# Performance work log

Hardware: AMD Instinct MI355X
Metric: run time of the kernel (lower is better)

The kernel has to match this reference:

```python
import jax, jax.numpy as jnp
import numpy as np

V = 128      # vocab size (pad=0, sos=1, eos=2)
E = 128      # embed_dim == LSTM hidden
L = 2        # rnn_layers
B = 8192     # batch (num_samples)
T = 128      # token sequence length incl. sos/eos
PAD, SOS, EOS = 0, 1, 2


def setup_inputs() -> dict:
    key = jax.random.key(0)
    ks = jax.random.split(key, 9)
    s = 1.0 / np.sqrt(E)
    state = jax.random.normal(ks[0], (B, E), dtype=jnp.float32)
    tokens = jax.random.randint(ks[1], (B, T), 3, V)
    tokens = tokens.at[:, 0].set(SOS).at[:, -1].set(EOS)
    tok_embed = jax.random.normal(ks[2], (V, E), dtype=jnp.float32)
    W_ih = jax.random.uniform(ks[3], (L, 4 * E, E), minval=-s, maxval=s, dtype=jnp.float32)
    W_hh = jax.random.uniform(ks[4], (L, 4 * E, E), minval=-s, maxval=s, dtype=jnp.float32)
    b_ih = jax.random.uniform(ks[5], (L, 4 * E), minval=-s, maxval=s, dtype=jnp.float32)
    b_hh = jax.random.uniform(ks[6], (L, 4 * E), minval=-s, maxval=s, dtype=jnp.float32)
    W_out = jax.random.uniform(ks[7], (V, E), minval=-s, maxval=s, dtype=jnp.float32)
    b_out = jax.random.uniform(ks[8], (V,), minval=-s, maxval=s, dtype=jnp.float32)
    return {"state": state, "tokens": tokens, "tok_embed": tok_embed,
            "W_ih": W_ih, "W_hh": W_hh, "b_ih": b_ih, "b_hh": b_hh,
            "W_out": W_out, "b_out": b_out}


def _lstm(x, h0, c0, W_ih, W_hh, b_ih, b_hh):
    # x: [T, B, E] time-major; h0/c0: [L, B, E]. Gate order i,f,g,o (torch).
    n_layers = W_ih.shape[0]
    hs, cs = [], []
    for l in range(n_layers):
        Wih, Whh = W_ih[l], W_hh[l]
        b = b_ih[l] + b_hh[l]
        def step(carry, xt, Wih=Wih, Whh=Whh, b=b):
            h, c = carry
            g = xt @ Wih.T + h @ Whh.T + b            # [B, 4E]
            i, f, gg, o = jnp.split(g, 4, axis=-1)
            c = jax.nn.sigmoid(f) * c + jax.nn.sigmoid(i) * jnp.tanh(gg)
            h = jax.nn.sigmoid(o) * jnp.tanh(c)
            return (h, c), h
        (h, c), x = jax.lax.scan(step, (h0[l], c0[l]), x)
        hs.append(h)
        cs.append(c)
    return x, jnp.stack(hs), jnp.stack(cs)


def reference(state, tokens, tok_embed, W_ih, W_hh, b_ih, b_hh, W_out, b_out):
    b, e = state.shape
    n_layers = W_ih.shape[0]
    zeros = jnp.zeros((n_layers, b, e), dtype=state.dtype)
    # get_init_state: one-step LSTM over state.unsqueeze(0)
    _, h0, c0 = _lstm(state[None], zeros, zeros, W_ih, W_hh, b_ih, b_hh)
    # get_likelihood (all sequences same length -> dense, no pad tokens)
    x = tok_embed[tokens.T]                               # [T, B, E]
    out, _, _ = _lstm(x, h0, c0, W_ih, W_hh, b_ih, b_hh)  # [T, B, E]
    logits = out[:-1] @ W_out.T + b_out                   # [T-1, B, V]
    targets = tokens.T[1:]                                # [T-1, B]
    lp = jax.nn.log_softmax(logits, axis=-1)
    nll = -jnp.take_along_axis(lp, targets[..., None], axis=-1)[..., 0]
    mask = (targets != PAD).astype(nll.dtype)             # ignore_index=pad
    ll = -jnp.sum(nll * mask, axis=0)[:, None]            # [B, 1]
    return ll
```

## Files before the change

kernel.cpp:

```cpp
#include <hip/hip_runtime.h>
#include <hip/hip_bf16.h>


typedef __bf16 bf16x8 __attribute__((ext_vector_type(8)));
typedef __bf16 bf16x4 __attribute__((ext_vector_type(4)));
typedef float  f32x4  __attribute__((ext_vector_type(4)));

#define LOG2E 1.4426950408889634f
#define LN2   0.6931471805599453f

static __device__ __bf16 g_emb1[128 * 512];
static __device__ __bf16 g_woutbf[128 * 128];
static __device__ __bf16 g_wih2bf[512 * 128];
static __device__ __bf16 g_h1[(size_t)128 * 8192 * 128];

__device__ __forceinline__ float frcp(float x) {
#if __has_builtin(__builtin_amdgcn_rcpf)
  return __builtin_amdgcn_rcpf(x);
#else
  return 1.0f / x;
#endif
}
__device__ __forceinline__ float fexp2(float x) {
#if __has_builtin(__builtin_amdgcn_exp2f)
  return __builtin_amdgcn_exp2f(x);
#else
  return exp2f(x);
#endif
}
__device__ __forceinline__ float flog2(float x) {
#if __has_builtin(__builtin_amdgcn_logf)
  return __builtin_amdgcn_logf(x);
#else
  return log2f(x);
#endif
}

__device__ __forceinline__ int hoff(int row, int e) {
  return row * 128 + ((e + ((row & 15) << 3)) & 127);
}

__global__ void prep_emb1(const float* __restrict__ emb, const float* __restrict__ Wih,
                          const float* __restrict__ bih, const float* __restrict__ bhh,
                          const float* __restrict__ Wout) {
  __shared__ float embS[128 * 128];
  __shared__ float wS[32 * 128];
  const int tid = threadIdx.x, bc = blockIdx.x;
  for (int i = tid; i < 128 * 32; i += 512) ((f32x4*)embS)[i] = ((const f32x4*)emb)[i];
  for (int i = tid; i < 32 * 32; i += 512)
    ((f32x4*)wS)[i] = ((const f32x4*)(Wih + bc * 32 * 128))[i];
  {
    int idx = bc * 512 + tid;
    g_woutbf[idx * 2]     = (__bf16)(Wout[idx * 2] * LOG2E);
    g_woutbf[idx * 2 + 1] = (__bf16)(Wout[idx * 2 + 1] * LOG2E);
  }
  for (int i = bc * 512 + tid; i < 512 * 128; i += 16 * 512) {
    int gate = (i >> 14) & 3;
    float sc = (gate == 2) ? 2.0f * LOG2E : LOG2E;
    g_wih2bf[i] = (__bf16)(Wih[512 * 128 + i] * sc);
  }
  __syncthreads();
  const int v = tid & 127, c0 = (tid >> 7) * 8;
  const int rot = v & 31;
#pragma unroll
  for (int j = 0; j < 8; ++j) {
    int c = c0 + j;
    float s = 0.f;
    for (int k = 0; k < 128; ++k) {
      int kk = (k + rot) & 127;
      s += embS[v * 128 + kk] * wS[c * 128 + kk];
    }
    int col = bc * 32 + c;
    float sc = ((col >> 7) == 2) ? 2.0f * LOG2E : LOG2E;
    g_emb1[v * 512 + col] = (__bf16)((s + bih[col] + bhh[col]) * sc);
  }
}

__global__ __launch_bounds__(512, 2) void lstm_l1(
    const float* __restrict__ state, const int* __restrict__ tokens,
    const float* __restrict__ W_ih, const float* __restrict__ W_hh,
    const float* __restrict__ b_ih, const float* __restrict__ b_hh) {
  __shared__ __align__(16) __bf16 whh1L[512 * 128];
  __shared__ __align__(16) __bf16 h1L[2][32 * 128];
  __shared__ unsigned char tokL[127][32];

  const int tid  = threadIdx.x;
  const int w    = tid >> 6;
  const int lane = tid & 63;
  const int lr   = lane & 15;
  const int lh   = lane >> 4;
  const int b0   = blockIdx.x * 32;
  const int col  = w * 16 + lr;
  const int koff = lh * 8;
  const int e0   = w * 16 + lh * 4;
  const float gscA[4] = {LOG2E, LOG2E, 2.0f * LOG2E, LOG2E};

  auto ldw8s = [&](const float* p, float sc) -> bf16x8 {
    f32x4 x0 = *(const f32x4*)p, x1 = *(const f32x4*)(p + 4);
    bf16x8 v;
#pragma unroll
    for (int j = 0; j < 4; ++j) { v[j] = (__bf16)(x0[j] * sc); v[4 + j] = (__bf16)(x1[j] * sc); }
    return v;
  };

  for (int i = tid; i < 512 * 16; i += 512) {
    int row = i >> 4, e = (i & 15) * 8;
    *(bf16x8*)(whh1L + hoff(row, e)) = ldw8s(W_hh + row * 128 + e, gscA[row >> 7]);
  }
  for (int i = tid; i < 127 * 32; i += 512) {
    int r = i & 31, t = i >> 5;
    tokL[t][r] = (unsigned char)tokens[(b0 + r) * 128 + t];
  }

  f32x4 acc[4][2];
  float c1[2][4] = {};

  auto ldB = [&](const __bf16* buf, int nf, int kc) -> bf16x8 {
    return *(const bf16x8*)(buf + hoff(nf * 16 + lr, kc * 32 + koff));
  };

  auto elem1 = [&](const f32x4* b4, __bf16* hout, __bf16* gout) {
#pragma unroll
    for (int nf = 0; nf < 2; ++nf) {
      bf16x4 hp;
#pragma unroll
      for (int j = 0; j < 4; ++j) {
        float gi = acc[0][nf][j] + b4[0][j];
        float gf = acc[1][nf][j] + b4[1][j];
        float gc = acc[2][nf][j] + b4[2][j];
        float go = acc[3][nf][j] + b4[3][j];
        float sf = frcp(1.f + fexp2(-gf));
        float si = frcp(1.f + fexp2(-gi));
        float tg = 1.f - 2.f * frcp(fexp2(gc) + 1.f);
        float cc = sf * c1[nf][j] + si * tg;
        c1[nf][j] = cc;
        float so = frcp(1.f + fexp2(-go));
        float tc = 1.f - 2.f * frcp(fexp2(2.f * LOG2E * cc) + 1.f);
        hp[j] = (__bf16)(so * tc);
      }
      int b = nf * 16 + lr;
      *(bf16x4*)(hout + hoff(b, e0)) = hp;
      *(bf16x4*)(gout + (size_t)(b0 + b) * 128 + e0) = hp;
    }
  };
  const f32x4 zf4 = {0.f, 0.f, 0.f, 0.f};
  const f32x4 zb4[4] = {zf4, zf4, zf4, zf4};

  __syncthreads();

  bf16x4 gv[2][4];
  auto gather = [&](int t) {
#pragma unroll
    for (int nf = 0; nf < 2; ++nf) {
      int tk = (int)tokL[t][nf * 16 + lr];
      const __bf16* pp = g_emb1 + tk * 512 + e0;
#pragma unroll
      for (int gg = 0; gg < 4; ++gg) gv[nf][gg] = *(const bf16x4*)(pp + gg * 128);
    }
  };
  gather(0);

  {
#pragma unroll
    for (int gg = 0; gg < 4; ++gg)
#pragma unroll
      for (int nf = 0; nf < 2; ++nf) acc[gg][nf] = zf4;
#pragma unroll
    for (int kc = 0; kc < 4; ++kc) {
      bf16x8 s0 = ldw8s(state + (size_t)(b0 + lr) * 128 + kc * 32 + koff, 1.0f);
      bf16x8 s1 = ldw8s(state + (size_t)(b0 + 16 + lr) * 128 + kc * 32 + koff, 1.0f);
#pragma unroll
      for (int gg = 0; gg < 4; ++gg) {
        bf16x8 a = ldw8s(W_ih + (gg * 128 + col) * 128 + kc * 32 + koff, gscA[gg]);
        acc[gg][0] = __builtin_amdgcn_mfma_f32_16x16x32_bf16(a, s0, acc[gg][0], 0, 0, 0);
        acc[gg][1] = __builtin_amdgcn_mfma_f32_16x16x32_bf16(a, s1, acc[gg][1], 0, 0, 0);
      }
    }
    f32x4 bias1v4[4];
#pragma unroll
    for (int gg = 0; gg < 4; ++gg)
#pragma unroll
      for (int j = 0; j < 4; ++j)
        bias1v4[gg][j] = (b_ih[gg * 128 + e0 + j] + b_hh[gg * 128 + e0 + j]) * gscA[gg];
    elem1(bias1v4, h1L[0], g_h1);
    __syncthreads();
  }

#pragma unroll 1
  for (int t = 0; t < 127; ++t) {
    const __bf16* h1p = h1L[t & 1];
    __bf16* h1c = h1L[(t & 1) ^ 1];
#pragma unroll
    for (int gg = 0; gg < 4; ++gg)
#pragma unroll
      for (int nf = 0; nf < 2; ++nf)
#pragma unroll
        for (int j = 0; j < 4; ++j) acc[gg][nf][j] = (float)gv[nf][gg][j];
#pragma unroll
    for (int kc = 0; kc < 4; ++kc) {
      bf16x8 p0 = ldB(h1p, 0, kc), p1 = ldB(h1p, 1, kc);
#pragma unroll
      for (int gg = 0; gg < 4; ++gg) {
        bf16x8 a = *(const bf16x8*)(whh1L + hoff(gg * 128 + col, kc * 32 + koff));
        acc[gg][0] = __builtin_amdgcn_mfma_f32_16x16x32_bf16(a, p0, acc[gg][0], 0, 0, 0);
        acc[gg][1] = __builtin_amdgcn_mfma_f32_16x16x32_bf16(a, p1, acc[gg][1], 0, 0, 0);
      }
    }
    if (t + 1 < 127) gather(t + 1);
    elem1(zb4, h1c, g_h1 + (size_t)(t + 1) * 8192 * 128);
    __syncthreads();
  }
}

__global__ __launch_bounds__(512, 2) void lstm_l2(
    const int* __restrict__ tokens, const float* __restrict__ W_hh,
    const float* __restrict__ b_ih, const float* __restrict__ b_hh,
    const float* __restrict__ b_out, float* __restrict__ out) {
  __shared__ __align__(16) __bf16 whh2L[512 * 128];
  __shared__ __align__(16) __bf16 h1S[32 * 128];
  __shared__ __align__(16) __bf16 h2L[2][32 * 128];
  __shared__ unsigned char tokL[128][32];
  __shared__ float wsum[8][32];
  __shared__ float llL[32];

  const int tid  = threadIdx.x;
  const int w    = tid >> 6;
  const int lane = tid & 63;
  const int lr   = lane & 15;
  const int lh   = lane >> 4;
  const int b0   = blockIdx.x * 32;
  const int col  = w * 16 + lr;
  const int koff = lh * 8;
  const int e0   = w * 16 + lh * 4;
  const float gscA[4] = {LOG2E, LOG2E, 2.0f * LOG2E, LOG2E};

  auto ldw8s = [&](const float* p, float sc) -> bf16x8 {
    f32x4 x0 = *(const f32x4*)p, x1 = *(const f32x4*)(p + 4);
    bf16x8 v;
#pragma unroll
    for (int j = 0; j < 4; ++j) { v[j] = (__bf16)(x0[j] * sc); v[4 + j] = (__bf16)(x1[j] * sc); }
    return v;
  };

  for (int i = tid; i < 512 * 16; i += 512) {
    int row = i >> 4, e = (i & 15) * 8;
    *(bf16x8*)(whh2L + hoff(row, e)) = ldw8s(W_hh + 512 * 128 + row * 128 + e, gscA[row >> 7]);
  }
  for (int i = tid; i < 128 * 32; i += 512) {
    int r = i & 31, t = i >> 5;
    tokL[t][r] = (unsigned char)tokens[(b0 + r) * 128 + t];
  }
  if (tid < 32) llL[tid] = 0.0f;

  auto stageH1 = [&](int slot) {
    const __bf16* src = g_h1 + (size_t)slot * 8192 * 128 + (size_t)b0 * 128;
    int r = tid >> 4, e = (tid & 15) * 8;
    bf16x8 v = *(const bf16x8*)(src + r * 128 + e);
    *(bf16x8*)(h1S + hoff(r, e)) = v;
  };
  stageH1(0);

  f32x4 bias2v4[4], bo4;
#pragma unroll
  for (int gg = 0; gg < 4; ++gg)
#pragma unroll
    for (int j = 0; j < 4; ++j)
      bias2v4[gg][j] = (b_ih[512 + gg * 128 + e0 + j] + b_hh[512 + gg * 128 + e0 + j]) * gscA[gg];
#pragma unroll
  for (int j = 0; j < 4; ++j) bo4[j] = b_out[e0 + j] * LOG2E;

  float c2[2][4] = {};
  f32x4 acc[4][2];

  auto ldB = [&](const __bf16* buf, int nf, int kc) -> bf16x8 {
    return *(const bf16x8*)(buf + hoff(nf * 16 + lr, kc * 32 + koff));
  };

  auto elem2 = [&](__bf16* hout) {
#pragma unroll
    for (int nf = 0; nf < 2; ++nf) {
      bf16x4 hp;
#pragma unroll
      for (int j = 0; j < 4; ++j) {
        float gi = acc[0][nf][j] + bias2v4[0][j];
        float gf = acc[1][nf][j] + bias2v4[1][j];
        float gc = acc[2][nf][j] + bias2v4[2][j];
        float go = acc[3][nf][j] + bias2v4[3][j];
        float sf = frcp(1.f + fexp2(-gf));
        float si = frcp(1.f + fexp2(-gi));
        float tg = 1.f - 2.f * frcp(fexp2(gc) + 1.f);
        float cc = sf * c2[nf][j] + si * tg;
        c2[nf][j] = cc;
        float so = frcp(1.f + fexp2(-go));
        float tc = 1.f - 2.f * frcp(fexp2(2.f * LOG2E * cc) + 1.f);
        hp[j] = (__bf16)(so * tc);
      }
      int b = nf * 16 + lr;
      *(bf16x4*)(hout + hoff(b, e0)) = hp;
    }
  };
  const f32x4 zf4 = {0.f, 0.f, 0.f, 0.f};

  __syncthreads();

  {
#pragma unroll
    for (int gg = 0; gg < 4; ++gg)
#pragma unroll
      for (int nf = 0; nf < 2; ++nf) acc[gg][nf] = zf4;
#pragma unroll
    for (int kc = 0; kc < 4; ++kc) {
      bf16x8 x0 = ldB(h1S, 0, kc), x1 = ldB(h1S, 1, kc);
#pragma unroll
      for (int gg = 0; gg < 4; ++gg) {
        bf16x8 a = *(const bf16x8*)(g_wih2bf + (size_t)(gg * 128 + col) * 128 + kc * 32 + koff);
        acc[gg][0] = __builtin_amdgcn_mfma_f32_16x16x32_bf16(a, x0, acc[gg][0], 0, 0, 0);
        acc[gg][1] = __builtin_amdgcn_mfma_f32_16x16x32_bf16(a, x1, acc[gg][1], 0, 0, 0);
      }
    }
    __syncthreads();
    elem2(h2L[1]);
    stageH1(1);
    __syncthreads();
  }

  f32x4 lvA, lvB;

#pragma unroll 1
  for (int t = 0; t <= 127; ++t) {
    const bool act = (t < 127), pend = (t > 0);
    const __bf16* prev = h2L[(t + 1) & 1];
    __bf16* cur = h2L[t & 1];

    f32x4 la0 = zf4, la1 = zf4;
    if (act) {
#pragma unroll
      for (int gg = 0; gg < 4; ++gg)
#pragma unroll
        for (int nf = 0; nf < 2; ++nf) acc[gg][nf] = zf4;
    }
#pragma unroll
    for (int kc = 0; kc < 4; ++kc) {
      if (act) {
        bf16x8 x0 = ldB(h1S, 0, kc), x1 = ldB(h1S, 1, kc);
#pragma unroll
        for (int gg = 0; gg < 4; ++gg) {
          bf16x8 a = *(const bf16x8*)(g_wih2bf + (size_t)(gg * 128 + col) * 128 + kc * 32 + koff);
          acc[gg][0] = __builtin_amdgcn_mfma_f32_16x16x32_bf16(a, x0, acc[gg][0], 0, 0, 0);
          acc[gg][1] = __builtin_amdgcn_mfma_f32_16x16x32_bf16(a, x1, acc[gg][1], 0, 0, 0);
        }
      }
      bf16x8 y0 = ldB(prev, 0, kc), y1 = ldB(prev, 1, kc);
      if (act) {
#pragma unroll
        for (int gg = 0; gg < 4; ++gg) {
          bf16x8 a2 = *(const bf16x8*)(whh2L + hoff(gg * 128 + col, kc * 32 + koff));
          acc[gg][0] = __builtin_amdgcn_mfma_f32_16x16x32_bf16(a2, y0, acc[gg][0], 0, 0, 0);
          acc[gg][1] = __builtin_amdgcn_mfma_f32_16x16x32_bf16(a2, y1, acc[gg][1], 0, 0, 0);
        }
      }
      if (pend) {
        bf16x8 wo = *(const bf16x8*)(g_woutbf + col * 128 + kc * 32 + koff);
        la0 = __builtin_amdgcn_mfma_f32_16x16x32_bf16(wo, y0, la0, 0, 0, 0);
        la1 = __builtin_amdgcn_mfma_f32_16x16x32_bf16(wo, y1, la1, 0, 0, 0);
      }
    }
    if (pend) {
      lvA = la0 + bo4;
      lvB = la1 + bo4;
      float s0 = fexp2(lvA[0]) + fexp2(lvA[1]) + fexp2(lvA[2]) + fexp2(lvA[3]);
      float s1 = fexp2(lvB[0]) + fexp2(lvB[1]) + fexp2(lvB[2]) + fexp2(lvB[3]);
      s0 += __shfl_xor(s0, 16); s0 += __shfl_xor(s0, 32);
      s1 += __shfl_xor(s1, 16); s1 += __shfl_xor(s1, 32);
      if (lh == 0) { wsum[w][lr] = s0; wsum[w][16 + lr] = s1; }
    }
    __syncthreads();

    if (pend) {
#pragma unroll
      for (int nf = 0; nf < 2; ++nf) {
        int r = nf * 16 + lr;
        int tgt = (int)tokL[t][r];
        if ((tgt >> 4) == w && ((tgt >> 2) & 3) == lh) {
          int j = tgt & 3;
          const f32x4& lv = nf ? lvB : lvA;
          float lvs = (j & 2) ? ((j & 1) ? lv[3] : lv[2]) : ((j & 1) ? lv[1] : lv[0]);
          float S = 0.f;
#pragma unroll
          for (int ww = 0; ww < 8; ++ww) S += wsum[ww][r];
          llL[r] += lvs - flog2(S);
        }
      }
    }
    if (act) elem2(cur);
    if (act && t <= 125) stageH1(t + 2);
    __syncthreads();
  }

  if (tid < 32) out[b0 + tid] = llL[tid] * LN2;
}

extern "C" void kernel_launch(void* const* d_in, const int* in_sizes, int n_in,
                              void* d_out, int out_size, void* d_ws, size_t ws_size,
                              hipStream_t stream) {
  const float* state  = (const float*)d_in[0];
  const int*   tokens = (const int*)d_in[1];
  const float* emb    = (const float*)d_in[2];
  const float* Wih    = (const float*)d_in[3];
  const float* Whh    = (const float*)d_in[4];
  const float* bih    = (const float*)d_in[5];
  const float* bhh    = (const float*)d_in[6];
  const float* Wout   = (const float*)d_in[7];
  const float* bout   = (const float*)d_in[8];
  float* out = (float*)d_out;

  prep_emb1<<<16, 512, 0, stream>>>(emb, Wih, bih, bhh, Wout);
  lstm_l1<<<256, 512, 0, stream>>>(state, tokens, Wih, Whh, bih, bhh);
  lstm_l2<<<256, 512, 0, stream>>>(tokens, Whh, bih, bhh, bout, out);
}
```

Before: 1.223 ms.

## Split layer-2 LSTM from logits/log-softmax into separate kernel via global h2 buffer

```diff
diff --git a/kernel.cpp b/kernel.cpp
--- a/kernel.cpp
+++ b/kernel.cpp
@@ -8,11 +8,14 @@
 
 #define LOG2E 1.4426950408889634f
 #define LN2   0.6931471805599453f
+
+#define LDS_BARRIER() asm volatile("s_waitcnt lgkmcnt(0)\n\ts_barrier" ::: "memory")
 
 static __device__ __bf16 g_emb1[128 * 512];
 static __device__ __bf16 g_woutbf[128 * 128];
 static __device__ __bf16 g_wih2bf[512 * 128];
 static __device__ __bf16 g_h1[(size_t)128 * 8192 * 128];
+static __device__ __bf16 g_h2[(size_t)127 * 8192 * 128];
 
 __device__ __forceinline__ float frcp(float x) {
 #if __has_builtin(__builtin_amdgcn_rcpf)
@@ -40,9 +43,9 @@
   return row * 128 + ((e + ((row & 15) << 3)) & 127);
 }
 
-__global__ void prep_emb1(const float* __restrict__ emb, const float* __restrict__ Wih,
-                          const float* __restrict__ bih, const float* __restrict__ bhh,
-                          const float* __restrict__ Wout) {
+__global__ void prep_tables(const float* __restrict__ emb, const float* __restrict__ Wih,
+                            const float* __restrict__ bih, const float* __restrict__ bhh,
+                            const float* __restrict__ Wout) {
   __shared__ float embS[128 * 128];
   __shared__ float wS[32 * 128];
   const int tid = threadIdx.x, bc = blockIdx.x;
@@ -183,7 +186,7 @@
       for (int j = 0; j < 4; ++j)
         bias1v4[gg][j] = (b_ih[gg * 128 + e0 + j] + b_hh[gg * 128 + e0 + j]) * gscA[gg];
     elem1(bias1v4, h1L[0], g_h1);
-    __syncthreads();
+    LDS_BARRIER();
   }
 
 #pragma unroll 1
@@ -208,20 +211,15 @@
     }
     if (t + 1 < 127) gather(t + 1);
     elem1(zb4, h1c, g_h1 + (size_t)(t + 1) * 8192 * 128);
-    __syncthreads();
-  }
-}
-
-__global__ __launch_bounds__(512, 2) void lstm_l2(
-    const int* __restrict__ tokens, const float* __restrict__ W_hh,
-    const float* __restrict__ b_ih, const float* __restrict__ b_hh,
-    const float* __restrict__ b_out, float* __restrict__ out) {
+    LDS_BARRIER();
+  }
+}
+
+__global__ __launch_bounds__(512, 2) void lstm_l2rec(
+    const float* __restrict__ W_hh, const float* __restrict__ b_ih,
+    const float* __restrict__ b_hh) {
   __shared__ __align__(16) __bf16 whh2L[512 * 128];
-  __shared__ __align__(16) __bf16 h1S[32 * 128];
   __shared__ __align__(16) __bf16 h2L[2][32 * 128];
-  __shared__ unsigned char tokL[128][32];
-  __shared__ float wsum[8][32];
-  __shared__ float llL[32];
 
   const int tid  = threadIdx.x;
   const int w    = tid >> 6;
@@ -246,28 +244,13 @@
     int row = i >> 4, e = (i & 15) * 8;
     *(bf16x8*)(whh2L + hoff(row, e)) = ldw8s(W_hh + 512 * 128 + row * 128 + e, gscA[row >> 7]);
   }
-  for (int i = tid; i < 128 * 32; i += 512) {
-    int r = i & 31, t = i >> 5;
-    tokL[t][r] = (unsigned char)tokens[(b0 + r) * 128 + t];
-  }
-  if (tid < 32) llL[tid] = 0.0f;
-
-  auto stageH1 = [&](int slot) {
-    const __bf16* src = g_h1 + (size_t)slot * 8192 * 128 + (size_t)b0 * 128;
-    int r = tid >> 4, e = (tid & 15) * 8;
-    bf16x8 v = *(const bf16x8*)(src + r * 128 + e);
-    *(bf16x8*)(h1S + hoff(r, e)) = v;
-  };
-  stageH1(0);
-
-  f32x4 bias2v4[4], bo4;
+
+  f32x4 bias2v4[4];
 #pragma unroll
   for (int gg = 0; gg < 4; ++gg)
 #pragma unroll
     for (int j = 0; j < 4; ++j)
       bias2v4[gg][j] = (b_ih[512 + gg * 128 + e0 + j] + b_hh[512 + gg * 128 + e0 + j]) * gscA[gg];
-#pragma unroll
-  for (int j = 0; j < 4; ++j) bo4[j] = b_out[e0 + j] * LOG2E;
 
   float c2[2][4] = {};
   f32x4 acc[4][2];
@@ -275,8 +258,12 @@
   auto ldB = [&](const __bf16* buf, int nf, int kc) -> bf16x8 {
     return *(const bf16x8*)(buf + hoff(nf * 16 + lr, kc * 32 + koff));
   };
-
-  auto elem2 = [&](__bf16* hout) {
+  auto ldX = [&](int slot, int nf, int kc) -> bf16x8 {
+    return *(const bf16x8*)(g_h1 + (size_t)slot * 8192 * 128 +
+                            (size_t)(b0 + nf * 16 + lr) * 128 + kc * 32 + koff);
+  };
+
+  auto elem2 = [&](__bf16* hout, __bf16* gout) {
 #pragma unroll
     for (int nf = 0; nf < 2; ++nf) {
       bf16x4 hp;
@@ -297,6 +284,7 @@
       }
       int b = nf * 16 + lr;
       *(bf16x4*)(hout + hoff(b, e0)) = hp;
+      if (gout) *(bf16x4*)(gout + (size_t)(b0 + b) * 128 + e0) = hp;
     }
   };
   const f32x4 zf4 = {0.f, 0.f, 0.f, 0.f};
@@ -310,7 +298,7 @@
       for (int nf = 0; nf < 2; ++nf) acc[gg][nf] = zf4;
 #pragma unroll
     for (int kc = 0; kc < 4; ++kc) {
-      bf16x8 x0 = ldB(h1S, 0, kc), x1 = ldB(h1S, 1, kc);
+      bf16x8 x0 = ldX(0, 0, kc), x1 = ldX(0, 1, kc);
 #pragma unroll
       for (int gg = 0; gg < 4; ++gg) {
         bf16x8 a = *(const bf16x8*)(g_wih2bf + (size_t)(gg * 128 + col) * 128 + kc * 32 + koff);
@@ -318,86 +306,131 @@
         acc[gg][1] = __builtin_amdgcn_mfma_f32_16x16x32_bf16(a, x1, acc[gg][1], 0, 0, 0);
       }
     }
-    __syncthreads();
-    elem2(h2L[1]);
-    stageH1(1);
-    __syncthreads();
-  }
-
-  f32x4 lvA, lvB;
+    elem2(h2L[0], nullptr);
+    LDS_BARRIER();
+  }
 
 #pragma unroll 1
-  for (int t = 0; t <= 127; ++t) {
-    const bool act = (t < 127), pend = (t > 0);
-    const __bf16* prev = h2L[(t + 1) & 1];
-    __bf16* cur = h2L[t & 1];
-
-    f32x4 la0 = zf4, la1 = zf4;
-    if (act) {
-#pragma unroll
-      for (int gg = 0; gg < 4; ++gg)
-#pragma unroll
-        for (int nf = 0; nf < 2; ++nf) acc[gg][nf] = zf4;
-    }
+  for (int t = 0; t < 127; ++t) {
+    const __bf16* prev = h2L[t & 1];
+    __bf16* cur = h2L[(t & 1) ^ 1];
+
+    bf16x8 x0[4], x1[4];
+#pragma unroll
+    for (int kc = 0; kc < 4; ++kc) { x0[kc] = ldX(t + 1, 0, kc); x1[kc] = ldX(t + 1, 1, kc); }
+
+#pragma unroll
+    for (int gg = 0; gg < 4; ++gg)
+#pragma unroll
+      for (int nf = 0; nf < 2; ++nf) acc[gg][nf] = zf4;
 #pragma unroll
     for (int kc = 0; kc < 4; ++kc) {
-      if (act) {
-        bf16x8 x0 = ldB(h1S, 0, kc), x1 = ldB(h1S, 1, kc);
-#pragma unroll
-        for (int gg = 0; gg < 4; ++gg) {
-          bf16x8 a = *(const bf16x8*)(g_wih2bf + (size_t)(gg * 128 + col) * 128 + kc * 32 + koff);
-          acc[gg][0] = __builtin_amdgcn_mfma_f32_16x16x32_bf16(a, x0, acc[gg][0], 0, 0, 0);
-          acc[gg][1] = __builtin_amdgcn_mfma_f32_16x16x32_bf16(a, x1, acc[gg][1], 0, 0, 0);
+      bf16x8 y0 = ldB(prev, 0, kc), y1 = ldB(prev, 1, kc);
+#pragma unroll
+      for (int gg = 0; gg < 4; ++gg) {
+        bf16x8 a2 = *(const bf16x8*)(whh2L + hoff(gg * 128 + col, kc * 32 + koff));
+        acc[gg][0] = __builtin_amdgcn_mfma_f32_16x16x32_bf16(a2, y0, acc[gg][0], 0, 0, 0);
+        acc[gg][1] = __builtin_amdgcn_mfma_f32_16x16x32_bf16(a2, y1, acc[gg][1], 0, 0, 0);
+      }
+    }
+#pragma unroll
+    for (int kc = 0; kc < 4; ++kc) {
+#pragma unroll
+      for (int gg = 0; gg < 4; ++gg) {
+        bf16x8 a = *(const bf16x8*)(g_wih2bf + (size_t)(gg * 128 + col) * 128 + kc * 32 + koff);
+        acc[gg][0] = __builtin_amdgcn_mfma_f32_16x16x32_bf16(a, x0[kc], acc[gg][0], 0, 0, 0);
+        acc[gg][1] = __builtin_amdgcn_mfma_f32_16x16x32_bf16(a, x1[kc], acc[gg][1], 0, 0, 0);
+      }
+    }
+    elem2(cur, g_h2 + (size_t)t * 8192 * 128);
+    LDS_BARRIER();
+  }
+}
+
+__global__ __launch_bounds__(512, 2) void logits_ll(
+    const int* __restrict__ tokens, const float* __restrict__ b_out,
+    float* __restrict__ out) {
+  __shared__ __align__(16) __bf16 woL[128 * 128];
+  __shared__ unsigned char tokL[128][32];
+  __shared__ float llpart[8][32];
+
+  const int tid  = threadIdx.x;
+  const int w    = tid >> 6;
+  const int lane = tid & 63;
+  const int lr   = lane & 15;
+  const int lh   = lane >> 4;
+  const int b0   = blockIdx.x * 32;
+  const int koff = lh * 8;
+
+  for (int i = tid; i < 128 * 16; i += 512) {
+    int row = i >> 4, e = (i & 15) * 8;
+    *(bf16x8*)(woL + hoff(row, e)) = *(const bf16x8*)(g_woutbf + row * 128 + e);
+  }
+  for (int i = tid; i < 128 * 32; i += 512) {
+    int r = i & 31, t = i >> 5;
+    tokL[t][r] = (unsigned char)tokens[(b0 + r) * 128 + t];
+  }
+
+  f32x4 bo8[8];
+#pragma unroll
+  for (int mf = 0; mf < 8; ++mf)
+#pragma unroll
+    for (int j = 0; j < 4; ++j) bo8[mf][j] = b_out[mf * 16 + lh * 4 + j] * LOG2E;
+
+  __syncthreads();
+
+  float ll0 = 0.f, ll1 = 0.f;
+
+#pragma unroll 1
+  for (int t = w; t < 127; t += 8) {
+#pragma unroll
+    for (int nf = 0; nf < 2; ++nf) {
+      f32x4 acc8[8];
+#pragma unroll
+      for (int mf = 0; mf < 8; ++mf) acc8[mf] = bo8[mf];
+#pragma unroll
+      for (int kc = 0; kc < 4; ++kc) {
+        bf16x8 y = *(const bf16x8*)(g_h2 + (size_t)t * 8192 * 128 +
+                                    (size_t)(b0 + nf * 16 + lr) * 128 + kc * 32 + koff);
+#pragma unroll
+        for (int mf = 0; mf < 8; ++mf) {
+          bf16x8 a = *(const bf16x8*)(woL + hoff(mf * 16 + lr, kc * 32 + koff));
+          acc8[mf] = __builtin_amdgcn_mfma_f32_16x16x32_bf16(a, y, acc8[mf], 0, 0, 0);
         }
       }
-      bf16x8 y0 = ldB(prev, 0, kc), y1 = ldB(prev, 1, kc);
-      if (act) {
-#pragma unroll
-        for (int gg = 0; gg < 4; ++gg) {
-          bf16x8 a2 = *(const bf16x8*)(whh2L + hoff(gg * 128 + col, kc * 32 + koff));
-          acc[gg][0] = __builtin_amdgcn_mfma_f32_16x16x32_bf16(a2, y0, acc[gg][0], 0, 0, 0);
-          acc[gg][1] = __builtin_amdgcn_mfma_f32_16x16x32_bf16(a2, y1, acc[gg][1], 0, 0, 0);
-        }
-      }
-      if (pend) {
-        bf16x8 wo = *(const bf16x8*)(g_woutbf + col * 128 + kc * 32 + koff);
-        la0 = __builtin_amdgcn_mfma_f32_16x16x32_bf16(wo, y0, la0, 0, 0, 0);
-        la1 = __builtin_amdgcn_mfma_f32_16x16x32_bf16(wo, y1, la1, 0, 0, 0);
-      }
-    }
-    if (pend) {
-      lvA = la0 + bo4;
-      lvB = la1 + bo4;
-      float s0 = fexp2(lvA[0]) + fexp2(lvA[1]) + fexp2(lvA[2]) + fexp2(lvA[3]);
-      float s1 = fexp2(lvB[0]) + fexp2(lvB[1]) + fexp2(lvB[2]) + fexp2(lvB[3]);
-      s0 += __shfl_xor(s0, 16); s0 += __shfl_xor(s0, 32);
-      s1 += __shfl_xor(s1, 16); s1 += __shfl_xor(s1, 32);
-      if (lh == 0) { wsum[w][lr] = s0; wsum[w][16 + lr] = s1; }
-    }
-    __syncthreads();
-
-    if (pend) {
-#pragma unroll
-      for (int nf = 0; nf < 2; ++nf) {
-        int r = nf * 16 + lr;
-        int tgt = (int)tokL[t][r];
-        if ((tgt >> 4) == w && ((tgt >> 2) & 3) == lh) {
-          int j = tgt & 3;
-          const f32x4& lv = nf ? lvB : lvA;
-          float lvs = (j & 2) ? ((j & 1) ? lv[3] : lv[2]) : ((j & 1) ? lv[1] : lv[0]);
-          float S = 0.f;
-#pragma unroll
-          for (int ww = 0; ww < 8; ++ww) S += wsum[ww][r];
-          llL[r] += lvs - flog2(S);
-        }
-      }
-    }
-    if (act) elem2(cur);
-    if (act && t <= 125) stageH1(t + 2);
-    __syncthreads();
-  }
-
-  if (tid < 32) out[b0 + tid] = llL[tid] * LN2;
+      float s = 0.f;
+#pragma unroll
+      for (int mf = 0; mf < 8; ++mf)
+#pragma unroll
+        for (int j = 0; j < 4; ++j) s += fexp2(acc8[mf][j]);
+      s += __shfl_xor(s, 16);
+      s += __shfl_xor(s, 32);
+      int tgt = (int)tokL[t + 1][nf * 16 + lr];
+      float contrib = 0.f;
+      if (((tgt >> 2) & 3) == lh) {
+        int j = tgt & 3;
+        float lvs = 0.f;
+#pragma unroll
+        for (int mf = 0; mf < 8; ++mf)
+          if ((tgt >> 4) == mf)
+            lvs = (j & 2) ? ((j & 1) ? acc8[mf][3] : acc8[mf][2])
+                          : ((j & 1) ? acc8[mf][1] : acc8[mf][0]);
+        contrib = lvs - flog2(s);
+      }
+      if (nf == 0) ll0 += contrib; else ll1 += contrib;
+    }
+  }
+
+  ll0 += __shfl_xor(ll0, 16); ll0 += __shfl_xor(ll0, 32);
+  ll1 += __shfl_xor(ll1, 16); ll1 += __shfl_xor(ll1, 32);
+  if (lh == 0) { llpart[w][lr] = ll0; llpart[w][16 + lr] = ll1; }
+  __syncthreads();
+  if (tid < 32) {
+    float s = 0.f;
+#pragma unroll
+    for (int ww = 0; ww < 8; ++ww) s += llpart[ww][tid];
+    out[b0 + tid] = s * LN2;
+  }
 }
 
 extern "C" void kernel_launch(void* const* d_in, const int* in_sizes, int n_in,
@@ -414,7 +447,8 @@
   const float* bout   = (const float*)d_in[8];
   float* out = (float*)d_out;
 
-  prep_emb1<<<16, 512, 0, stream>>>(emb, Wih, bih, bhh, Wout);
+  prep_tables<<<16, 512, 0, stream>>>(emb, Wih, bih, bhh, Wout);
   lstm_l1<<<256, 512, 0, stream>>>(state, tokens, Wih, Whh, bih, bhh);
-  lstm_l2<<<256, 512, 0, stream>>>(tokens, Whh, bih, bhh, bout, out);
-}
+  lstm_l2rec<<<256, 512, 0, stream>>>(Whh, bih, bhh);
+  logits_ll<<<256, 512, 0, stream>>>(tokens, bout, out);
+}
```

After: 1.310 ms. +7.1%, slower.
